# Optimization experiments

Measured on AMD Instinct MI355X. Metric: run time of the kernel, lower is better.

Reference implementation:

```python
import jax, jax.numpy as jnp
import numpy as np

E4M3_MAX = 448.0  # max representable value of float8_e4m3fn


def _updated_scale(amax_history, amax_now, scale):
    # roll history, insert current amax, take running max (delayed scaling)
    hist = jnp.roll(amax_history, 1).at[0].set(amax_now)
    amax = jnp.max(hist)
    sf = E4M3_MAX / amax  # scale factor (margin = 0)
    sf = jnp.where((amax > 0.0) & jnp.isfinite(amax), sf, 1.0 / scale)
    return 1.0 / sf  # dequant scale


def _qdq(x, scale, amax_history):
    # quantize-dequantize through float8_e4m3fn with dynamic amax-history scaling
    amax_now = jnp.max(jnp.abs(x)).astype(jnp.float32)
    s = _updated_scale(amax_history, amax_now, scale[0])
    q = jnp.clip(x / s, -E4M3_MAX, E4M3_MAX).astype(jnp.float8_e4m3fn)
    return q.astype(x.dtype) * s


def setup_inputs() -> dict:
    key = jax.random.key(0)
    k1, k2 = jax.random.split(key, 2)
    B, S, D, F = 4, 2048, 4096, 16384
    HL = 16  # amax_history_length
    inputs = jax.random.normal(k1, (B, S, D), jnp.float32)
    # lecun_normal: std = 1/sqrt(fan_in)
    kernel = jax.random.normal(k2, (D, F), jnp.float32) * (1.0 / np.sqrt(D))
    bias = jnp.zeros((F,), jnp.float32)
    return {
        "inputs": inputs,
        "kernel": kernel,
        "bias": bias,
        "input_scale": jnp.ones((1,), jnp.float32),
        "input_amax_history": jnp.zeros((HL,), jnp.float32),
        "kernel_scale": jnp.ones((1,), jnp.float32),
        "kernel_amax_history": jnp.zeros((HL,), jnp.float32),
        "output_grad_scale": jnp.ones((1,), jnp.float32),
        "output_grad_amax_history": jnp.zeros((HL,), jnp.float32),
    }


def reference(inputs, kernel, bias, input_scale, input_amax_history,
              kernel_scale, kernel_amax_history, output_grad_scale,
              output_grad_amax_history):
    B, S, D = inputs.shape
    x = inputs.reshape(-1, D)  # (B*S, D)
    q_x = _qdq(x, input_scale, input_amax_history)
    q_k = _qdq(kernel, kernel_scale, kernel_amax_history)
    out = q_x @ q_k  # (B*S, F)
    # bias is rounded fp32->bf16->fp32 per the module
    b = bias.astype(jnp.bfloat16).astype(jnp.float32)
    out = jax.nn.gelu(out + b)
    return out.reshape(B, S, -1)
```

## Files before the change

kernel.cpp:

```cpp
#include <hip/hip_runtime.h>
#include <hip/hip_bf16.h>

typedef __attribute__((ext_vector_type(4))) int i32x4;
typedef __attribute__((ext_vector_type(8))) int i32x8;
typedef __attribute__((ext_vector_type(16))) float f32x16;

#define E4M3_MAX 448.0f
#define AS1 __attribute__((address_space(1)))
#define AS3 __attribute__((address_space(3)))

__device__ __forceinline__ float clip448(float v) {
  return fminf(fmaxf(v, -E4M3_MAX), E4M3_MAX);
}

__device__ __forceinline__ void gld_lds16(const void* g, void* l) {
  __builtin_amdgcn_global_load_lds((const AS1 void*)g, (AS3 void*)l, 16, 0, 0);
}

__global__ void init_ws_kernel(unsigned int* amax) {
  amax[0] = 0u;
  amax[1] = 0u;
}

__global__ void amax_kernel(const float* __restrict__ x, long n4,
                            unsigned int* __restrict__ amax_out) {
  long i0 = (long)blockIdx.x * blockDim.x + threadIdx.x;
  long stride = (long)gridDim.x * blockDim.x;
  const float4* x4 = (const float4*)x;
  float m = 0.f;
  for (long i = i0; i < n4; i += stride) {
    float4 v = x4[i];
    m = fmaxf(m, fmaxf(fmaxf(fabsf(v.x), fabsf(v.y)), fmaxf(fabsf(v.z), fabsf(v.w))));
  }
#pragma unroll
  for (int off = 32; off >= 1; off >>= 1)
    m = fmaxf(m, __shfl_xor(m, off));
  __shared__ float wmax[8];
  int wid = threadIdx.x >> 6;
  if ((threadIdx.x & 63) == 0) wmax[wid] = m;
  __syncthreads();
  if (threadIdx.x == 0) {
    int nw = blockDim.x >> 6;
    float bm = wmax[0];
    for (int w = 1; w < nw; ++w) bm = fmaxf(bm, wmax[w]);
    atomicMax(amax_out, __float_as_uint(bm));
  }
}

__global__ void scale_kernel(const unsigned int* __restrict__ amax,
                             const float* __restrict__ scale_x,
                             const float* __restrict__ hist_x,
                             const float* __restrict__ scale_k,
                             const float* __restrict__ hist_k,
                             int hl, float* __restrict__ scales) {
  if (threadIdx.x != 0) return;
  float ax = __uint_as_float(amax[0]);
  for (int i = 0; i < hl - 1; ++i) ax = fmaxf(ax, hist_x[i]);
  float sfx = E4M3_MAX / ax;
  if (!(ax > 0.f && isfinite(ax))) sfx = 1.f / scale_x[0];
  float sx = 1.f / sfx;
  float ak = __uint_as_float(amax[1]);
  for (int i = 0; i < hl - 1; ++i) ak = fmaxf(ak, hist_k[i]);
  float sfk = E4M3_MAX / ak;
  if (!(ak > 0.f && isfinite(ak))) sfk = 1.f / scale_k[0];
  float sk = 1.f / sfk;
  scales[0] = sx;
  scales[1] = sk;
  scales[2] = sx * sk;
}


__global__ void quant_x_kernel(const float* __restrict__ x,
                               unsigned char* __restrict__ Aq,
                               const float* __restrict__ scales, int K) {
  const float s = scales[0];
  const int kt = blockIdx.x, mt = blockIdx.y, nkt = gridDim.x;
  __shared__ float lt[128][68];
  const int t = threadIdx.x;
  const float* src = x + (size_t)mt * 128 * K + (size_t)kt * 64;
#pragma unroll
  for (int it = 0; it < 8; ++it) {
    int row = it * 16 + (t >> 4);
    int c4 = (t & 15) * 4;
    float4 v = *(const float4*)&src[(size_t)row * K + c4];
    lt[row][c4 + 0] = v.x; lt[row][c4 + 1] = v.y;
    lt[row][c4 + 2] = v.z; lt[row][c4 + 3] = v.w;
  }
  __syncthreads();
  uint4* out = (uint4*)(Aq + ((size_t)mt * nkt + kt) * 8192);
#pragma unroll
  for (int cc = 0; cc < 2; ++cc) {
    int c = t * 2 + cc;
    int g = c >> 7, h = (c >> 6) & 1, l = c & 63;
    int row = g * 32 + (l & 31);
    int kb = (l >> 5) * 32 + h * 16;
    unsigned int w[4];
#pragma unroll
    for (int q = 0; q < 4; ++q) {
      int b = kb + q * 4;
      int p = 0;
      p = __builtin_amdgcn_cvt_pk_fp8_f32(clip448(lt[row][b+0] / s), clip448(lt[row][b+1] / s), p, false);
      p = __builtin_amdgcn_cvt_pk_fp8_f32(clip448(lt[row][b+2] / s), clip448(lt[row][b+3] / s), p, true);
      w[q] = (unsigned int)p;
    }
    out[c] = make_uint4(w[0], w[1], w[2], w[3]);
  }
}

__global__ void quant_k_kernel(const float* __restrict__ w,
                               unsigned char* __restrict__ Bq,
                               const float* __restrict__ scales, int N) {
  const float s = scales[1];
  const int kt = blockIdx.x, nt = blockIdx.y, nkt = gridDim.x;
  __shared__ float lt[64][132];
  const int t = threadIdx.x;
  const float* src = w + (size_t)kt * 64 * N + (size_t)nt * 128;
#pragma unroll
  for (int it = 0; it < 8; ++it) {
    int row = it * 8 + (t >> 5);
    int c4 = (t & 31) * 4;
    float4 v = *(const float4*)&src[(size_t)row * N + c4];
    lt[row][c4 + 0] = v.x; lt[row][c4 + 1] = v.y;
    lt[row][c4 + 2] = v.z; lt[row][c4 + 3] = v.w;
  }
  __syncthreads();
  uint4* out = (uint4*)(Bq + ((size_t)nt * nkt + kt) * 8192);
#pragma unroll
  for (int cc = 0; cc < 2; ++cc) {
    int c = t * 2 + cc;
    int g = c >> 7, h = (c >> 6) & 1, l = c & 63;
    int nl = g * 32 + (l & 31);
    int kb = (l >> 5) * 32 + h * 16;
    unsigned int w4[4];
#pragma unroll
    for (int q = 0; q < 4; ++q) {
      int b = kb + q * 4;
      int p = 0;
      p = __builtin_amdgcn_cvt_pk_fp8_f32(clip448(lt[b+0][nl] / s), clip448(lt[b+1][nl] / s), p, false);
      p = __builtin_amdgcn_cvt_pk_fp8_f32(clip448(lt[b+2][nl] / s), clip448(lt[b+3][nl] / s), p, true);
      w4[q] = (unsigned int)p;
    }
    out[c] = make_uint4(w4[0], w4[1], w4[2], w4[3]);
  }
}

__global__ __launch_bounds__(256, 3) void gemm_fp8_kernel(
    const unsigned char* __restrict__ Aq, const unsigned char* __restrict__ Bq,
    const float* __restrict__ bias, const float* __restrict__ scales,
    float* __restrict__ C, int M, int N, int K) {
  __shared__ __align__(16) unsigned char lA[8192];
  __shared__ __align__(16) unsigned char lB[8192];
  const float s_xk = scales[2];
  const int nkt = K >> 6;
  const int t = threadIdx.x;
  const int lane = t & 63;
  const int wid = t >> 6;
  const int wm = wid >> 1, wn = wid & 1;

  const unsigned char* ga = Aq + (size_t)blockIdx.y * nkt * 8192 + t * 16;
  const unsigned char* gb = Bq + (size_t)blockIdx.x * nkt * 8192 + t * 16;

  f32x16 acc[2][2];
#pragma unroll
  for (int i = 0; i < 2; ++i)
#pragma unroll
    for (int j = 0; j < 2; ++j)
#pragma unroll
      for (int r = 0; r < 16; ++r) acc[i][j][r] = 0.f;

  for (int kt = 0; kt < nkt; ++kt) {
    gld_lds16(ga,        &lA[wid * 1024]);
    gld_lds16(ga + 4096, &lA[wid * 1024 + 4096]);
    gld_lds16(gb,        &lB[wid * 1024]);
    gld_lds16(gb + 4096, &lB[wid * 1024 + 4096]);
    ga += 8192;
    gb += 8192;
    __syncthreads();

    i32x8 av[2], bv[2];
#pragma unroll
    for (int i = 0; i < 2; ++i) {
      int base = (wm * 2 + i) * 2048 + lane * 16;
      i32x4 lo = *(const i32x4*)&lA[base];
      i32x4 hi = *(const i32x4*)&lA[base + 1024];
      av[i] = __builtin_shufflevector(lo, hi, 0, 1, 2, 3, 4, 5, 6, 7);
    }
#pragma unroll
    for (int j = 0; j < 2; ++j) {
      int base = (wn * 2 + j) * 2048 + lane * 16;
      i32x4 lo = *(const i32x4*)&lB[base];
      i32x4 hi = *(const i32x4*)&lB[base + 1024];
      bv[j] = __builtin_shufflevector(lo, hi, 0, 1, 2, 3, 4, 5, 6, 7);
    }

#pragma unroll
    for (int i = 0; i < 2; ++i)
#pragma unroll
      for (int j = 0; j < 2; ++j)
        acc[i][j] = __builtin_amdgcn_mfma_scale_f32_32x32x64_f8f6f4(
            av[i], bv[j], acc[i][j], 0, 0, 0, 127, 0, 127);
    __syncthreads();
  }

  const int m0 = blockIdx.y * 128;
  const int n0 = blockIdx.x * 128;
  float bb[2];
#pragma unroll
  for (int j = 0; j < 2; ++j) {
    int col = n0 + wn * 64 + j * 32 + (lane & 31);
    bb[j] = __bfloat162float(__float2bfloat16(bias[col]));
  }
#pragma unroll
  for (int i = 0; i < 2; ++i) {
    int rowbase = m0 + wm * 64 + i * 32 + 4 * (lane >> 5);
#pragma unroll
    for (int j = 0; j < 2; ++j) {
      int col = n0 + wn * 64 + j * 32 + (lane & 31);
#pragma unroll
      for (int r = 0; r < 16; ++r) {
        int row = rowbase + (r & 3) + 8 * (r >> 2);
        float v = acc[i][j][r] * s_xk + bb[j];
        float g = 0.5f * v *
                  (1.0f + tanhf(0.7978845608028654f * (v + 0.044715f * v * v * v)));
        C[(size_t)row * N + col] = g;
      }
    }
  }
}

extern "C" void kernel_launch(void* const* d_in, const int* in_sizes, int n_in,
                              void* d_out, int out_size, void* d_ws, size_t ws_size,
                              hipStream_t stream) {
  const float* inputs = (const float*)d_in[0];
  const float* kernelw = (const float*)d_in[1];
  const float* bias = (const float*)d_in[2];
  const float* input_scale = (const float*)d_in[3];
  const float* input_hist = (const float*)d_in[4];
  const float* kernel_scale = (const float*)d_in[5];
  const float* kernel_hist = (const float*)d_in[6];

  const int F = in_sizes[2];
  const int D = in_sizes[1] / F;
  const long M = (long)in_sizes[0] / D;
  const int HL = in_sizes[4];
  const int N = F, K = D;

  unsigned int* amax = (unsigned int*)d_ws;
  float* scales = (float*)((char*)d_ws + 16);
  unsigned char* Aq = (unsigned char*)d_ws + 64;
  unsigned char* Bq = Aq + (size_t)M * K;

  float* C = (float*)d_out;

  init_ws_kernel<<<1, 1, 0, stream>>>(amax);
  amax_kernel<<<2048, 256, 0, stream>>>(inputs, (long)M * K / 4, &amax[0]);
  amax_kernel<<<2048, 256, 0, stream>>>(kernelw, (long)K * N / 4, &amax[1]);
  scale_kernel<<<1, 64, 0, stream>>>(amax, input_scale, input_hist, kernel_scale,
                                     kernel_hist, HL, scales);
  quant_x_kernel<<<dim3(K / 64, M / 128), 256, 0, stream>>>(inputs, Aq, scales, K);
  quant_k_kernel<<<dim3(K / 64, N / 128), 256, 0, stream>>>(kernelw, Bq, scales, N);
  gemm_fp8_kernel<<<dim3(N / 128, M / 128), 256, 0, stream>>>(Aq, Bq, bias, scales, C,
                                                              (int)M, N, K);
}
```

Measured before the change: 845.8 us.

## Enlarge GEMM tile to 256x256 with double-buffered LDS and swizzled block order

```diff
diff --git a/kernel.cpp b/kernel.cpp
--- a/kernel.cpp
+++ b/kernel.cpp
@@ -15,6 +15,15 @@
 
 __device__ __forceinline__ void gld_lds16(const void* g, void* l) {
   __builtin_amdgcn_global_load_lds((const AS1 void*)g, (AS3 void*)l, 16, 0, 0);
+}
+
+__device__ __forceinline__ float gelu_f(float v) {
+  float y = 0.7978845608028654f * (v + 0.044715f * v * v * v);
+  float a = fabsf(y);
+  float z = __expf(-2.f * a);
+  float th = (1.f - z) / (1.f + z);
+  th = copysignf(th, y);
+  return 0.5f * v * (1.f + th);
 }
 
 __global__ void init_ws_kernel(unsigned int* amax) {
@@ -144,66 +153,92 @@
   }
 }
 
-__global__ __launch_bounds__(256, 3) void gemm_fp8_kernel(
+__global__ __launch_bounds__(512, 2) void gemm_fp8_kernel(
     const unsigned char* __restrict__ Aq, const unsigned char* __restrict__ Bq,
     const float* __restrict__ bias, const float* __restrict__ scales,
     float* __restrict__ C, int M, int N, int K) {
-  __shared__ __align__(16) unsigned char lA[8192];
-  __shared__ __align__(16) unsigned char lB[8192];
+  __shared__ __align__(16) unsigned char lds[65536];
   const float s_xk = scales[2];
   const int nkt = K >> 6;
   const int t = threadIdx.x;
   const int lane = t & 63;
   const int wid = t >> 6;
-  const int wm = wid >> 1, wn = wid & 1;
-
-  const unsigned char* ga = Aq + (size_t)blockIdx.y * nkt * 8192 + t * 16;
-  const unsigned char* gb = Bq + (size_t)blockIdx.x * nkt * 8192 + t * 16;
-
-  f32x16 acc[2][2];
-#pragma unroll
-  for (int i = 0; i < 2; ++i)
+  const int wm = wid >> 2, wn = wid & 3;
+
+  int f = blockIdx.y * gridDim.x + blockIdx.x;
+  int cpx = (gridDim.x * gridDim.y) >> 3;
+  int f2 = (f & 7) * cpx + (f >> 3);
+  int bx = f2 % gridDim.x;
+  int by = f2 / gridDim.x;
+
+  const size_t strideT = (size_t)nkt * 8192;
+  const unsigned char* gA = Aq + (size_t)(2 * by) * strideT + t * 16;
+  const unsigned char* gB = Bq + (size_t)(2 * bx) * strideT + t * 16;
+
+  f32x16 acc[4][2];
+#pragma unroll
+  for (int i = 0; i < 4; ++i)
 #pragma unroll
     for (int j = 0; j < 2; ++j)
 #pragma unroll
       for (int r = 0; r < 16; ++r) acc[i][j][r] = 0.f;
 
-  for (int kt = 0; kt < nkt; ++kt) {
-    gld_lds16(ga,        &lA[wid * 1024]);
-    gld_lds16(ga + 4096, &lA[wid * 1024 + 4096]);
-    gld_lds16(gb,        &lB[wid * 1024]);
-    gld_lds16(gb + 4096, &lB[wid * 1024 + 4096]);
-    ga += 8192;
-    gb += 8192;
-    __syncthreads();
-
-    i32x8 av[2], bv[2];
-#pragma unroll
-    for (int i = 0; i < 2; ++i) {
-      int base = (wm * 2 + i) * 2048 + lane * 16;
-      i32x4 lo = *(const i32x4*)&lA[base];
-      i32x4 hi = *(const i32x4*)&lA[base + 1024];
+  auto stage = [&](int buf, int kt_) {
+    size_t o = (size_t)kt_ * 8192;
+    unsigned char* l = lds + buf * 32768 + wid * 1024;
+    gld_lds16(gA + o,           l);
+    gld_lds16(gA + strideT + o, l + 8192);
+    gld_lds16(gB + o,           l + 16384);
+    gld_lds16(gB + strideT + o, l + 24576);
+  };
+
+  auto compute = [&](int buf) {
+    const unsigned char* la = lds + buf * 32768;
+    const unsigned char* lb = la + 16384;
+    i32x8 av[4], bv[2];
+#pragma unroll
+    for (int i = 0; i < 4; ++i) {
+      int g = wm * 4 + i;
+      i32x4 lo = *(const i32x4*)&la[g * 2048 + lane * 16];
+      i32x4 hi = *(const i32x4*)&la[g * 2048 + 1024 + lane * 16];
       av[i] = __builtin_shufflevector(lo, hi, 0, 1, 2, 3, 4, 5, 6, 7);
     }
 #pragma unroll
     for (int j = 0; j < 2; ++j) {
-      int base = (wn * 2 + j) * 2048 + lane * 16;
-      i32x4 lo = *(const i32x4*)&lB[base];
-      i32x4 hi = *(const i32x4*)&lB[base + 1024];
+      int g = wn * 2 + j;
+      i32x4 lo = *(const i32x4*)&lb[g * 2048 + lane * 16];
+      i32x4 hi = *(const i32x4*)&lb[g * 2048 + 1024 + lane * 16];
       bv[j] = __builtin_shufflevector(lo, hi, 0, 1, 2, 3, 4, 5, 6, 7);
     }
-
-#pragma unroll
-    for (int i = 0; i < 2; ++i)
+    __builtin_amdgcn_s_setprio(1);
+#pragma unroll
+    for (int i = 0; i < 4; ++i)
 #pragma unroll
       for (int j = 0; j < 2; ++j)
         acc[i][j] = __builtin_amdgcn_mfma_scale_f32_32x32x64_f8f6f4(
             av[i], bv[j], acc[i][j], 0, 0, 0, 127, 0, 127);
-    __syncthreads();
-  }
-
-  const int m0 = blockIdx.y * 128;
-  const int n0 = blockIdx.x * 128;
+    __builtin_amdgcn_s_setprio(0);
+  };
+
+  stage(0, 0);
+  int buf = 0;
+  for (int kt = 0; kt < nkt - 1; ++kt) {
+    stage(buf ^ 1, kt + 1);
+    asm volatile("s_waitcnt vmcnt(4)" ::: "memory");
+    __builtin_amdgcn_s_barrier();
+    asm volatile("" ::: "memory");
+    compute(buf);
+    asm volatile("" ::: "memory");
+    __builtin_amdgcn_s_barrier();
+    buf ^= 1;
+  }
+  asm volatile("s_waitcnt vmcnt(0)" ::: "memory");
+  __builtin_amdgcn_s_barrier();
+  asm volatile("" ::: "memory");
+  compute(buf);
+
+  const int m0 = by * 256;
+  const int n0 = bx * 256;
   float bb[2];
 #pragma unroll
   for (int j = 0; j < 2; ++j) {
@@ -211,8 +246,8 @@
     bb[j] = __bfloat162float(__float2bfloat16(bias[col]));
   }
 #pragma unroll
-  for (int i = 0; i < 2; ++i) {
-    int rowbase = m0 + wm * 64 + i * 32 + 4 * (lane >> 5);
+  for (int i = 0; i < 4; ++i) {
+    int rowbase = m0 + wm * 128 + i * 32 + 4 * (lane >> 5);
 #pragma unroll
     for (int j = 0; j < 2; ++j) {
       int col = n0 + wn * 64 + j * 32 + (lane & 31);
@@ -220,9 +255,7 @@
       for (int r = 0; r < 16; ++r) {
         int row = rowbase + (r & 3) + 8 * (r >> 2);
         float v = acc[i][j][r] * s_xk + bb[j];
-        float g = 0.5f * v *
-                  (1.0f + tanhf(0.7978845608028654f * (v + 0.044715f * v * v * v)));
-        C[(size_t)row * N + col] = g;
+        C[(size_t)row * N + col] = gelu_f(v);
       }
     }
   }
@@ -259,6 +292,6 @@
                                      kernel_hist, HL, scales);
   quant_x_kernel<<<dim3(K / 64, M / 128), 256, 0, stream>>>(inputs, Aq, scales, K);
   quant_k_kernel<<<dim3(K / 64, N / 128), 256, 0, stream>>>(kernelw, Bq, scales, N);
-  gemm_fp8_kernel<<<dim3(N / 128, M / 128), 256, 0, stream>>>(Aq, Bq, bias, scales, C,
+  gemm_fp8_kernel<<<dim3(N / 256, M / 256), 512, 0, stream>>>(Aq, Bq, bias, scales, C,
                                                               (int)M, N, K);
 }
```

Result: faster. 779.0 us (-7.9%).
